# Performance work log

Hardware: AMD Instinct MI355X
Metric: run time of the kernel (lower is better)

## Reference

```python
import jax, jax.numpy as jnp
import numpy as np

N = 50000
E = 600000
D = 128  # embedding_dimension


def _lrelu(x):
    return jax.nn.leaky_relu(x, negative_slope=0.01)


def _rgcn(x, edge_index, edge_type, rel_w, root_w, bias):
    # FastRGCNConv, num_relations=2, aggr='mean' (PyG default).
    # Compute per-relation transforms as 2 dense GEMMs, then gather per edge.
    h = jnp.einsum('nd,rde->rne', x, rel_w)          # [2, N, D]
    src, dst = edge_index[0], edge_index[1]
    msg = h[edge_type, src]                          # [E, D] gather
    agg = jax.ops.segment_sum(msg, dst, num_segments=x.shape[0])
    deg = jax.ops.segment_sum(jnp.ones((msg.shape[0],), x.dtype), dst,
                              num_segments=x.shape[0])
    agg = agg / jnp.maximum(deg, 1.0)[:, None]       # mean over in-edges
    return agg + x @ root_w + bias


def setup_inputs() -> dict:
    key = jax.random.key(0)
    ks = jax.random.split(key, 32)
    f32 = jnp.float32
    inp = {
        'des': jax.random.normal(ks[0], (N, 768), f32),
        'tweet': jax.random.normal(ks[1], (N, 768), f32),
        'num_prop': jax.random.normal(ks[2], (N, 7), f32),
        'cat_prop': jax.random.normal(ks[3], (N, 11), f32),
        'new_feature': jax.random.normal(ks[4], (N, 1), f32),
        'edge_index': jax.random.randint(ks[5], (2, E), 0, N),
        'edge_type': jax.random.randint(ks[6], (E,), 0, 2),
    }
    def lin(k, i, o, s=0.05):
        kw, kb = jax.random.split(k)
        return (jax.random.normal(kw, (i, o), f32) * s,
                jax.random.normal(kb, (o,), f32) * s)
    pf = D // 5  # 25
    inp['W_des'], inp['b_des'] = lin(ks[7], 768, pf)
    inp['W_tweet'], inp['b_tweet'] = lin(ks[8], 768, 28)
    inp['W_num'], inp['b_num'] = lin(ks[9], 7, pf)
    inp['W_cat'], inp['b_cat'] = lin(ks[10], 11, pf)
    inp['W_new'], inp['b_new'] = lin(ks[11], 1, pf)
    inp['W_in'], inp['b_in'] = lin(ks[12], D, D)
    inp['rel_w1'] = jax.random.normal(ks[13], (2, D, D), f32) * 0.05
    inp['root_w1'] = jax.random.normal(ks[14], (D, D), f32) * 0.05
    inp['bias1'] = jax.random.normal(ks[15], (D,), f32) * 0.05
    inp['rel_w2'] = jax.random.normal(ks[16], (2, D, D), f32) * 0.05
    inp['root_w2'] = jax.random.normal(ks[17], (D, D), f32) * 0.05
    inp['bias2'] = jax.random.normal(ks[18], (D,), f32) * 0.05
    inp['W_out1'], inp['b_out1'] = lin(ks[19], D, D)
    inp['W_out2'], inp['b_out2'] = lin(ks[20], D, 2)
    return inp


def reference(des, tweet, num_prop, cat_prop, new_feature,
              W_des, b_des, W_tweet, b_tweet, W_num, b_num,
              W_cat, b_cat, W_new, b_new, W_in, b_in,
              rel_w1, root_w1, bias1, rel_w2, root_w2, bias2,
              W_out1, b_out1, W_out2, b_out2,
              edge_index, edge_type):
    d = _lrelu(des @ W_des + b_des)
    t = _lrelu(tweet @ W_tweet + b_tweet)
    n = _lrelu(num_prop @ W_num + b_num)
    c = _lrelu(cat_prop @ W_cat + b_cat)
    nf = _lrelu(new_feature @ W_new + b_new)
    x = jnp.concatenate((d, t, n, c, nf), axis=1)  # [N, 128]
    x = _lrelu(x @ W_in + b_in)
    x = _rgcn(x, edge_index, edge_type, rel_w1, root_w1, bias1)
    # dropout is identity at eval time
    x = _rgcn(x, edge_index, edge_type, rel_w2, root_w2, bias2)
    x = _lrelu(x @ W_out1 + b_out1)
    return x @ W_out2 + b_out2  # [N, 2]
```

## Files before the change

### kernel.cpp

```cpp
#include <hip/hip_runtime.h>

#define N_NODES 50000
#define N_EDGES 600000
#define NPAD    50048
#define NBLK_SCAN 196

static __device__ __forceinline__ float lrelu(float v) {
    return v > 0.f ? v : 0.01f * v;
}

template<int NCOLS>
__global__ __launch_bounds__(256) void proj768_v2(
    const float* __restrict__ A, const float* __restrict__ W,
    float* __restrict__ P)
{
    const int row = blockIdx.x * 256 + threadIdx.x;
    const int kh  = blockIdx.y;
    if (row >= N_NODES) return;
    float acc[NCOLS];
    #pragma unroll
    for (int c = 0; c < NCOLS; c++) acc[c] = 0.f;

    const float4* Ar = (const float4*)(A + (size_t)row * 768 + (size_t)kh * 384);
    const float*  Wp = W + (size_t)kh * 384 * NCOLS;

    #pragma unroll 2
    for (int k4 = 0; k4 < 96; k4++) {
        float4 a = Ar[k4];
        const float* w = Wp + k4 * 4 * NCOLS;
        #pragma unroll
        for (int c = 0; c < NCOLS; c++)
            acc[c] += a.x * w[c] + a.y * w[NCOLS + c]
                    + a.z * w[2 * NCOLS + c] + a.w * w[3 * NCOLS + c];
    }
    float* o = P + ((size_t)kh * N_NODES + row) * 32;
    #pragma unroll
    for (int c = 0; c < NCOLS; c++) o[c] = acc[c];
}

__global__ void combine_proj(const float* __restrict__ P,
                             const float* __restrict__ bd, const float* __restrict__ bt,
                             float* __restrict__ X0)
{
    int id = blockIdx.x * 256 + threadIdx.x;
    int n = id >> 6, c = id & 63;
    if (n >= N_NODES || c >= 53) return;
    const float* Pd = P;
    const float* Pt = P + (size_t)2 * N_NODES * 32;
    float v; int col;
    if (c < 25) {
        v = Pd[(size_t)n * 32 + c] + Pd[((size_t)N_NODES + n) * 32 + c] + bd[c];
        col = c;
    } else {
        int cc = c - 25;
        v = Pt[(size_t)n * 32 + cc] + Pt[((size_t)N_NODES + n) * 32 + cc] + bt[cc];
        col = 25 + cc;
    }
    X0[(size_t)n * 128 + col] = lrelu(v);
}

__global__ void small_proj_kernel(
    const float* __restrict__ nump, const float* __restrict__ catp, const float* __restrict__ newf,
    const float* __restrict__ Wn, const float* __restrict__ bn,
    const float* __restrict__ Wc, const float* __restrict__ bc,
    const float* __restrict__ Ww, const float* __restrict__ bw,
    float* __restrict__ out)
{
    int id = blockIdx.x * 256 + threadIdx.x;
    int n = id / 75, c = id % 75;
    if (n >= N_NODES) return;
    float acc; int col;
    if (c < 25) {
        col = 53 + c; acc = bn[c];
        #pragma unroll
        for (int k = 0; k < 7; k++) acc += nump[n * 7 + k] * Wn[k * 25 + c];
    } else if (c < 50) {
        int cc = c - 25; col = 78 + cc; acc = bc[cc];
        #pragma unroll
        for (int k = 0; k < 11; k++) acc += catp[n * 11 + k] * Wc[k * 25 + cc];
    } else {
        int cc = c - 50; col = 103 + cc;
        acc = bw[cc] + newf[n] * Ww[cc];
    }
    out[(size_t)n * 128 + col] = lrelu(acc);
}

template<int KTOT, bool SPLIT, bool ACT>
__global__ __launch_bounds__(256, 4) void gemm_v2(
    const float* __restrict__ A, const float* __restrict__ A2,
    const float* __restrict__ B, const float* __restrict__ B2,
    const float* __restrict__ bias, float* __restrict__ out)
{
    __shared__ float AlT[32 * 132];
    __shared__ float Bl [32 * 132];
    const int t  = threadIdx.x;
    const int r0 = blockIdx.x * 128;
    const int tx = t & 15, ty = t >> 4;

    float acc[8][8] = {};

    for (int k0 = 0; k0 < KTOT; k0 += 32) {
        #pragma unroll
        for (int i = 0; i < 4; i++) {
            int f4i = t + i * 256;
            int row = f4i >> 3, c4 = f4i & 7;
            int k = k0 + c4 * 4;
            float4 v;
            if (!SPLIT) {
                v = *(const float4*)&A[(size_t)(r0 + row) * 128 + k];
            } else {
                if (k < 256) v = *(const float4*)&A[(size_t)(r0 + row) * 256 + k];
                else         v = *(const float4*)&A2[(size_t)(r0 + row) * 128 + (k - 256)];
            }
            AlT[(c4 * 4 + 0) * 132 + row] = v.x;
            AlT[(c4 * 4 + 1) * 132 + row] = v.y;
            AlT[(c4 * 4 + 2) * 132 + row] = v.z;
            AlT[(c4 * 4 + 3) * 132 + row] = v.w;
        }
        #pragma unroll
        for (int i = 0; i < 4; i++) {
            int f4i = t + i * 256;
            int kk = f4i >> 5, c4 = f4i & 31;
            int k = k0 + kk;
            float4 v;
            if (!SPLIT) v = *(const float4*)&B[(size_t)k * 128 + c4 * 4];
            else v = (k < 256) ? *(const float4*)&B[(size_t)k * 128 + c4 * 4]
                               : *(const float4*)&B2[(size_t)(k - 256) * 128 + c4 * 4];
            *(float4*)&Bl[kk * 132 + c4 * 4] = v;
        }
        __syncthreads();
        #pragma unroll 4
        for (int k = 0; k < 32; k++) {
            float4 a0 = *(const float4*)&AlT[k * 132 + ty * 8];
            float4 a1 = *(const float4*)&AlT[k * 132 + ty * 8 + 4];
            float4 b0 = *(const float4*)&Bl [k * 132 + tx * 8];
            float4 b1 = *(const float4*)&Bl [k * 132 + tx * 8 + 4];
            float av[8] = {a0.x, a0.y, a0.z, a0.w, a1.x, a1.y, a1.z, a1.w};
            float bv[8] = {b0.x, b0.y, b0.z, b0.w, b1.x, b1.y, b1.z, b1.w};
            #pragma unroll
            for (int i = 0; i < 8; i++)
                #pragma unroll
                for (int j = 0; j < 8; j++) acc[i][j] += av[i] * bv[j];
        }
        __syncthreads();
    }
    float4 bb0 = *(const float4*)&bias[tx * 8];
    float4 bb1 = *(const float4*)&bias[tx * 8 + 4];
    float bb[8] = {bb0.x, bb0.y, bb0.z, bb0.w, bb1.x, bb1.y, bb1.z, bb1.w};
    #pragma unroll
    for (int i = 0; i < 8; i++) {
        size_t row = (size_t)(r0 + ty * 8 + i);
        float o[8];
        #pragma unroll
        for (int j = 0; j < 8; j++) {
            o[j] = acc[i][j] + bb[j];
            if (ACT) o[j] = lrelu(o[j]);
        }
        *(float4*)&out[row * 128 + tx * 8]     = make_float4(o[0], o[1], o[2], o[3]);
        *(float4*)&out[row * 128 + tx * 8 + 4] = make_float4(o[4], o[5], o[6], o[7]);
    }
}

__global__ void count_kernel(const int* __restrict__ ei, int* __restrict__ count) {
    int e = blockIdx.x * 256 + threadIdx.x;
    if (e < N_EDGES) atomicAdd(&count[ei[N_EDGES + e]], 1);
}

__global__ void scan1_kernel(const int* __restrict__ count, int* __restrict__ partial) {
    __shared__ int sm[256];
    int b = blockIdx.x, t = threadIdx.x;
    int i = b * 256 + t;
    sm[t] = (i < N_NODES) ? count[i] : 0;
    __syncthreads();
    for (int off = 128; off > 0; off >>= 1) {
        if (t < off) sm[t] += sm[t + off];
        __syncthreads();
    }
    if (t == 0) partial[b] = sm[0];
}

__global__ void scan2_kernel(int* __restrict__ partial) {
    __shared__ int sm[256];
    int t = threadIdx.x;
    int v = (t < NBLK_SCAN) ? partial[t] : 0;
    sm[t] = v; __syncthreads();
    for (int off = 1; off < 256; off <<= 1) {
        int add = (t >= off) ? sm[t - off] : 0;
        __syncthreads();
        sm[t] += add;
        __syncthreads();
    }
    partial[t] = sm[t] - v;
}

__global__ void scan3_kernel(const int* __restrict__ count, const int* __restrict__ partial,
                             int* __restrict__ offsets) {
    __shared__ int sm[256];
    int b = blockIdx.x, t = threadIdx.x;
    int i = b * 256 + t;
    int v = (i < N_NODES) ? count[i] : 0;
    sm[t] = v; __syncthreads();
    for (int off = 1; off < 256; off <<= 1) {
        int add = (t >= off) ? sm[t - off] : 0;
        __syncthreads();
        sm[t] += add;
        __syncthreads();
    }
    if (i < N_NODES) offsets[i] = partial[b] + sm[t] - v;
}

__global__ void fill_kernel(const int* __restrict__ ei, const int* __restrict__ et,
                            const int* __restrict__ offsets, int* __restrict__ cursor,
                            int* __restrict__ elist) {
    int e = blockIdx.x * 256 + threadIdx.x;
    if (e < N_EDGES) {
        int d = ei[N_EDGES + e];
        int pos = atomicAdd(&cursor[d], 1);
        elist[offsets[d] + pos] = (int)(((unsigned)ei[e]) | (((unsigned)et[e]) << 31));
    }
}

__global__ __launch_bounds__(256) void aggregate_v2(
    const float* __restrict__ x, const int* __restrict__ offsets,
    const int* __restrict__ count, const int* __restrict__ elist,
    float* __restrict__ s)
{
    int nid  = blockIdx.x * 8 + (threadIdx.x >> 5);
    int lane = threadIdx.x & 31;
    if (nid >= N_NODES) return;
    int start = offsets[nid], dg = count[nid];
    float4 a0 = make_float4(0.f, 0.f, 0.f, 0.f);
    float4 a1 = make_float4(0.f, 0.f, 0.f, 0.f);
    for (int i = 0; i < dg; i++) {
        int v = elist[start + i];
        const float4* xr = (const float4*)&x[(size_t)(v & 0x7FFFFFFF) * 128];
        float4 val = xr[lane];
        if (v < 0) { a1.x += val.x; a1.y += val.y; a1.z += val.z; a1.w += val.w; }
        else       { a0.x += val.x; a0.y += val.y; a0.z += val.z; a0.w += val.w; }
    }
    float inv = 1.0f / (float)(dg > 0 ? dg : 1);
    a0.x *= inv; a0.y *= inv; a0.z *= inv; a0.w *= inv;
    a1.x *= inv; a1.y *= inv; a1.z *= inv; a1.w *= inv;
    ((float4*)&s[(size_t)nid * 256])[lane]       = a0;
    ((float4*)&s[(size_t)nid * 256 + 128])[lane] = a1;
}

__global__ __launch_bounds__(64) void final_kernel(
    const float* __restrict__ x, const float* __restrict__ W2,
    const float* __restrict__ b2, float* __restrict__ out)
{
    int n = blockIdx.x;
    int t = threadIdx.x;
    float x0 = x[(size_t)n * 128 + t];
    float x1 = x[(size_t)n * 128 + 64 + t];
    float p0 = x0 * W2[t * 2]     + x1 * W2[(t + 64) * 2];
    float p1 = x0 * W2[t * 2 + 1] + x1 * W2[(t + 64) * 2 + 1];
    #pragma unroll
    for (int off = 32; off > 0; off >>= 1) {
        p0 += __shfl_down(p0, off);
        p1 += __shfl_down(p1, off);
    }
    if (t == 0) {
        out[(size_t)n * 2]     = p0 + b2[0];
        out[(size_t)n * 2 + 1] = p1 + b2[1];
    }
}

extern "C" void kernel_launch(void* const* d_in, const int* in_sizes, int n_in,
                              void* d_out, int out_size, void* d_ws, size_t ws_size,
                              hipStream_t stream)
{
    const float* des   = (const float*)d_in[0];
    const float* tw    = (const float*)d_in[1];
    const float* nump  = (const float*)d_in[2];
    const float* catp  = (const float*)d_in[3];
    const float* newf  = (const float*)d_in[4];
    const int*   ei    = (const int*)d_in[5];
    const int*   et    = (const int*)d_in[6];
    const float* Wd    = (const float*)d_in[7];  const float* bd  = (const float*)d_in[8];
    const float* Wt    = (const float*)d_in[9];  const float* bt  = (const float*)d_in[10];
    const float* Wn    = (const float*)d_in[11]; const float* bn  = (const float*)d_in[12];
    const float* Wc    = (const float*)d_in[13]; const float* bc  = (const float*)d_in[14];
    const float* Ww    = (const float*)d_in[15]; const float* bw  = (const float*)d_in[16];
    const float* Win   = (const float*)d_in[17]; const float* bin = (const float*)d_in[18];
    const float* relw1 = (const float*)d_in[19]; const float* rootw1 = (const float*)d_in[20];
    const float* bias1 = (const float*)d_in[21];
    const float* relw2 = (const float*)d_in[22]; const float* rootw2 = (const float*)d_in[23];
    const float* bias2 = (const float*)d_in[24];
    const float* Wo1   = (const float*)d_in[25]; const float* bo1 = (const float*)d_in[26];
    const float* Wo2   = (const float*)d_in[27]; const float* bo2 = (const float*)d_in[28];
    float* outp = (float*)d_out;

    char* ws = (char*)d_ws;
    const size_t szX = (size_t)NPAD * 128 * sizeof(float);
    float* X0 = (float*)(ws);
    float* X1 = (float*)(ws + szX);
    float* S  = (float*)(ws + 2 * szX);
    float* P  = S;
    char* p = ws + 2 * szX + (size_t)NPAD * 256 * sizeof(float);
    int* count   = (int*)p; p += (size_t)NPAD * 4;
    int* offsets = (int*)p; p += (size_t)NPAD * 4;
    int* cursor  = (int*)p; p += (size_t)NPAD * 4;
    int* elist   = (int*)p; p += (size_t)N_EDGES * 4;
    int* partial = (int*)p;

    hipMemsetAsync(count,  0, NPAD * sizeof(int), stream);
    hipMemsetAsync(cursor, 0, NPAD * sizeof(int), stream);

    dim3 pg((N_NODES + 255) / 256, 2);
    proj768_v2<25><<<pg, 256, 0, stream>>>(des, Wd, P);
    proj768_v2<28><<<pg, 256, 0, stream>>>(tw, Wt, P + (size_t)2 * N_NODES * 32);
    small_proj_kernel<<<(N_NODES * 75 + 255) / 256, 256, 0, stream>>>(
        nump, catp, newf, Wn, bn, Wc, bc, Ww, bw, X0);
    combine_proj<<<(N_NODES * 64 + 255) / 256, 256, 0, stream>>>(P, bd, bt, X0);
    gemm_v2<128, false, true><<<NPAD / 128, 256, 0, stream>>>(
        X0, nullptr, Win, nullptr, bin, X1);

    count_kernel<<<(N_EDGES + 255) / 256, 256, 0, stream>>>(ei, count);
    scan1_kernel<<<NBLK_SCAN, 256, 0, stream>>>(count, partial);
    scan2_kernel<<<1, 256, 0, stream>>>(partial);
    scan3_kernel<<<NBLK_SCAN, 256, 0, stream>>>(count, partial, offsets);
    fill_kernel<<<(N_EDGES + 255) / 256, 256, 0, stream>>>(ei, et, offsets, cursor, elist);

    aggregate_v2<<<(N_NODES + 7) / 8, 256, 0, stream>>>(X1, offsets, count, elist, S);
    gemm_v2<384, true, false><<<NPAD / 128, 256, 0, stream>>>(
        S, X1, relw1, rootw1, bias1, X0);

    aggregate_v2<<<(N_NODES + 7) / 8, 256, 0, stream>>>(X0, offsets, count, elist, S);
    gemm_v2<384, true, false><<<NPAD / 128, 256, 0, stream>>>(
        S, X0, relw2, rootw2, bias2, X1);

    gemm_v2<128, false, true><<<NPAD / 128, 256, 0, stream>>>(
        X1, nullptr, Wo1, nullptr, bo1, X0);
    final_kernel<<<N_NODES, 64, 0, stream>>>(X0, Wo2, bo2, outp);
}
```

Measured before the change: 979.4 us.

## Fuse 768-wide projection split-K reduction in shared memory and unroll aggregation

The 768-input projections now split K four ways inside a block (64 rows by 4 K-quarters), reduce the partials through padded shared memory, and write biased leaky-ReLU output directly into X0. This removes the global partial buffer and the separate combine_proj launch. The edge aggregation loop is also unrolled by two so that two neighbour row gathers are in flight at once. The cost is more shared memory per block (which may limit occupancy) and fewer rows per block in the projection.

```diff
diff --git a/kernel.cpp b/kernel.cpp
--- a/kernel.cpp
+++ b/kernel.cpp
@@ -10,53 +10,55 @@
 }
 
 template<int NCOLS>
-__global__ __launch_bounds__(256) void proj768_v2(
+__global__ __launch_bounds__(256) void proj768_v3(
     const float* __restrict__ A, const float* __restrict__ W,
-    float* __restrict__ P)
-{
-    const int row = blockIdx.x * 256 + threadIdx.x;
-    const int kh  = blockIdx.y;
-    if (row >= N_NODES) return;
+    const float* __restrict__ bias, int coff, float* __restrict__ X0)
+{
+    constexpr int PAD = (NCOLS % 2 == 0) ? NCOLS + 1 : NCOLS;
+    __shared__ float red[4 * 64 * PAD];
+    const int t    = threadIdx.x;
+    const int lane = t & 63;
+    const int kh   = t >> 6;
+    const int r0   = blockIdx.x * 64;
+    const int row  = r0 + lane;
+    const int rowc = row < N_NODES ? row : N_NODES - 1;
+
     float acc[NCOLS];
     #pragma unroll
     for (int c = 0; c < NCOLS; c++) acc[c] = 0.f;
 
-    const float4* Ar = (const float4*)(A + (size_t)row * 768 + (size_t)kh * 384);
-    const float*  Wp = W + (size_t)kh * 384 * NCOLS;
+    const float4* Ar = (const float4*)(A + (size_t)rowc * 768 + kh * 192);
+    const float*  Wp = W + (size_t)kh * 192 * NCOLS;
 
     #pragma unroll 2
-    for (int k4 = 0; k4 < 96; k4++) {
-        float4 a = Ar[k4];
-        const float* w = Wp + k4 * 4 * NCOLS;
+    for (int j = 0; j < 48; j++) {
+        float4 a = Ar[j];
+        const float* w = Wp + j * 4 * NCOLS;
         #pragma unroll
         for (int c = 0; c < NCOLS; c++)
             acc[c] += a.x * w[c] + a.y * w[NCOLS + c]
                     + a.z * w[2 * NCOLS + c] + a.w * w[3 * NCOLS + c];
     }
-    float* o = P + ((size_t)kh * N_NODES + row) * 32;
+
+    float* rd = &red[(kh * 64 + lane) * PAD];
     #pragma unroll
-    for (int c = 0; c < NCOLS; c++) o[c] = acc[c];
-}
-
-__global__ void combine_proj(const float* __restrict__ P,
-                             const float* __restrict__ bd, const float* __restrict__ bt,
-                             float* __restrict__ X0)
-{
-    int id = blockIdx.x * 256 + threadIdx.x;
-    int n = id >> 6, c = id & 63;
-    if (n >= N_NODES || c >= 53) return;
-    const float* Pd = P;
-    const float* Pt = P + (size_t)2 * N_NODES * 32;
-    float v; int col;
-    if (c < 25) {
-        v = Pd[(size_t)n * 32 + c] + Pd[((size_t)N_NODES + n) * 32 + c] + bd[c];
-        col = c;
-    } else {
-        int cc = c - 25;
-        v = Pt[(size_t)n * 32 + cc] + Pt[((size_t)N_NODES + n) * 32 + cc] + bt[cc];
-        col = 25 + cc;
-    }
-    X0[(size_t)n * 128 + col] = lrelu(v);
+    for (int c = 0; c < NCOLS; c++) rd[c] = acc[c];
+    __syncthreads();
+
+    const int c  = t & 31;
+    const int rb = t >> 5;
+    if (c < NCOLS) {
+        float bc = bias[c];
+        #pragma unroll
+        for (int rr = 0; rr < 8; rr++) {
+            int r = rb + rr * 8;
+            float s = red[(0 * 64 + r) * PAD + c] + red[(1 * 64 + r) * PAD + c]
+                    + red[(2 * 64 + r) * PAD + c] + red[(3 * 64 + r) * PAD + c];
+            int n = r0 + r;
+            if (n < N_NODES)
+                X0[(size_t)n * 128 + coff + c] = lrelu(s + bc);
+        }
+    }
 }
 
 __global__ void small_proj_kernel(
@@ -220,7 +222,7 @@
     }
 }
 
-__global__ __launch_bounds__(256) void aggregate_v2(
+__global__ __launch_bounds__(256) void aggregate_v3(
     const float* __restrict__ x, const int* __restrict__ offsets,
     const int* __restrict__ count, const int* __restrict__ elist,
     float* __restrict__ s)
@@ -231,12 +233,22 @@
     int start = offsets[nid], dg = count[nid];
     float4 a0 = make_float4(0.f, 0.f, 0.f, 0.f);
     float4 a1 = make_float4(0.f, 0.f, 0.f, 0.f);
-    for (int i = 0; i < dg; i++) {
-        int v = elist[start + i];
-        const float4* xr = (const float4*)&x[(size_t)(v & 0x7FFFFFFF) * 128];
-        float4 val = xr[lane];
-        if (v < 0) { a1.x += val.x; a1.y += val.y; a1.z += val.z; a1.w += val.w; }
-        else       { a0.x += val.x; a0.y += val.y; a0.z += val.z; a0.w += val.w; }
+    int i = 0;
+    for (; i + 2 <= dg; i += 2) {
+        int v0 = elist[start + i];
+        int v1 = elist[start + i + 1];
+        float4 u = ((const float4*)&x[(size_t)(v0 & 0x7FFFFFFF) * 128])[lane];
+        float4 w = ((const float4*)&x[(size_t)(v1 & 0x7FFFFFFF) * 128])[lane];
+        if (v0 < 0) { a1.x += u.x; a1.y += u.y; a1.z += u.z; a1.w += u.w; }
+        else        { a0.x += u.x; a0.y += u.y; a0.z += u.z; a0.w += u.w; }
+        if (v1 < 0) { a1.x += w.x; a1.y += w.y; a1.z += w.z; a1.w += w.w; }
+        else        { a0.x += w.x; a0.y += w.y; a0.z += w.z; a0.w += w.w; }
+    }
+    if (i < dg) {
+        int v0 = elist[start + i];
+        float4 u = ((const float4*)&x[(size_t)(v0 & 0x7FFFFFFF) * 128])[lane];
+        if (v0 < 0) { a1.x += u.x; a1.y += u.y; a1.z += u.z; a1.w += u.w; }
+        else        { a0.x += u.x; a0.y += u.y; a0.z += u.z; a0.w += u.w; }
     }
     float inv = 1.0f / (float)(dg > 0 ? dg : 1);
     a0.x *= inv; a0.y *= inv; a0.z *= inv; a0.w *= inv;
@@ -296,7 +308,6 @@
     float* X0 = (float*)(ws);
     float* X1 = (float*)(ws + szX);
     float* S  = (float*)(ws + 2 * szX);
-    float* P  = S;
     char* p = ws + 2 * szX + (size_t)NPAD * 256 * sizeof(float);
     int* count   = (int*)p; p += (size_t)NPAD * 4;
     int* offsets = (int*)p; p += (size_t)NPAD * 4;
@@ -307,12 +318,10 @@
     hipMemsetAsync(count,  0, NPAD * sizeof(int), stream);
     hipMemsetAsync(cursor, 0, NPAD * sizeof(int), stream);
 
-    dim3 pg((N_NODES + 255) / 256, 2);
-    proj768_v2<25><<<pg, 256, 0, stream>>>(des, Wd, P);
-    proj768_v2<28><<<pg, 256, 0, stream>>>(tw, Wt, P + (size_t)2 * N_NODES * 32);
+    proj768_v3<25><<<NPAD / 64, 256, 0, stream>>>(des, Wd, bd, 0,  X0);
+    proj768_v3<28><<<NPAD / 64, 256, 0, stream>>>(tw,  Wt, bt, 25, X0);
     small_proj_kernel<<<(N_NODES * 75 + 255) / 256, 256, 0, stream>>>(
         nump, catp, newf, Wn, bn, Wc, bc, Ww, bw, X0);
-    combine_proj<<<(N_NODES * 64 + 255) / 256, 256, 0, stream>>>(P, bd, bt, X0);
     gemm_v2<128, false, true><<<NPAD / 128, 256, 0, stream>>>(
         X0, nullptr, Win, nullptr, bin, X1);
 
@@ -322,11 +331,11 @@
     scan3_kernel<<<NBLK_SCAN, 256, 0, stream>>>(count, partial, offsets);
     fill_kernel<<<(N_EDGES + 255) / 256, 256, 0, stream>>>(ei, et, offsets, cursor, elist);
 
-    aggregate_v2<<<(N_NODES + 7) / 8, 256, 0, stream>>>(X1, offsets, count, elist, S);
+    aggregate_v3<<<(N_NODES + 7) / 8, 256, 0, stream>>>(X1, offsets, count, elist, S);
     gemm_v2<384, true, false><<<NPAD / 128, 256, 0, stream>>>(
         S, X1, relw1, rootw1, bias1, X0);
 
-    aggregate_v2<<<(N_NODES + 7) / 8, 256, 0, stream>>>(X0, offsets, count, elist, S);
+    aggregate_v3<<<(N_NODES + 7) / 8, 256, 0, stream>>>(X0, offsets, count, elist, S);
     gemm_v2<384, true, false><<<NPAD / 128, 256, 0, stream>>>(
         S, X0, relw2, rootw2, bias2, X1);
 
```

Measured after the change: 1.114 ms. 13.7% more time.
